# Performance work log

Hardware: AMD Instinct MI355X
Metric: run time of the kernel (lower is better)

## Reference

```python
import jax, jax.numpy as jnp
import numpy as np


def setup_inputs() -> dict:
    key = jax.random.key(0)
    k1, k2, k3 = jax.random.split(key, 3)
    N, C_in, H, W = 32, 16, 256, 256
    C_out, K = 64, 3
    x = jax.random.normal(k1, (N, C_in, H, W), dtype=jnp.float32)
    # match nn.Conv2d default init scale roughly (values irrelevant for correctness harness)
    fan_in = C_in * K * K
    bound = 1.0 / np.sqrt(fan_in)
    conv_weight = jax.random.normal(k2, (C_out, C_in, K, K), dtype=jnp.float32) * bound
    conv_bias = jax.random.normal(k3, (C_out,), dtype=jnp.float32) * bound
    return {"x": x, "conv_weight": conv_weight, "conv_bias": conv_bias}


def reference(x, conv_weight, conv_bias):
    # Conv2d: stride=1, padding=0 (VALID), dilation=1, groups=1
    y = jax.lax.conv_general_dilated(
        x, conv_weight,
        window_strides=(1, 1), padding='VALID',
        dimension_numbers=('NCHW', 'OIHW', 'NCHW'),
    ) + conv_bias[None, :, None, None]          # (N, C_out, OH, OW)
    y = jnp.min(y, axis=1, keepdims=True)       # min over output channels -> (N, 1, OH, OW)
    return jnp.tanh(jnp.tanh(y))                # double tanh
```

## Files before the change

kernel.cpp:

```cpp
#include <hip/hip_runtime.h>
#include <hip/hip_bf16.h>

typedef __attribute__((ext_vector_type(8)))  short short8;
typedef __attribute__((ext_vector_type(4)))  float f32x4;
typedef __attribute__((ext_vector_type(16))) float f32x16;

#define CIN   16
#define COUT  64
#define HH    256
#define WW    256
#define OHH   254
#define OWW   254

#define HSTR   (36 * 8)
#define HALF   (34 * HSTR + 8)

__device__ __forceinline__ ushort f2bf(float f) {
    unsigned u = __builtin_bit_cast(unsigned, f);
    unsigned r = (u + 0x7fffu + ((u >> 16) & 1u)) >> 16;
    return (ushort)r;
}

__device__ __forceinline__ float dtanh2(float x) {
    const float K = 2.8853900817779268f;
    float xc = fminf(fmaxf(x, -9.0f), 9.0f);
    float e1 = __builtin_amdgcn_exp2f(K * xc);
    float t1 = 1.0f - 2.0f * __builtin_amdgcn_rcpf(e1 + 1.0f);
    float e2 = __builtin_amdgcn_exp2f(K * t1);
    return 1.0f - 2.0f * __builtin_amdgcn_rcpf(e2 + 1.0f);
}

__global__ void prep_weights(const float* __restrict__ wsrc, ushort* __restrict__ wfrag) {
    int idx = blockIdx.x * 256 + threadIdx.x;
    if (idx >= 9216) return;
    int r    = idx & 7;
    int lane = (idx >> 3) & 63;
    int j    = (idx >> 9) & 1;
    int tap  = idx >> 10;
    int ci   = 8 * (lane >> 5) + r;
    int co   = j * 32 + (lane & 31);
    int kh   = tap / 3, kw = tap - 3 * kh;
    wfrag[idx] = f2bf(wsrc[(co * CIN + ci) * 9 + kh * 3 + kw]);
}

__global__ __launch_bounds__(256, 3) void conv_min_tanh(
        const float* __restrict__ x, const ushort* __restrict__ wfrag,
        const float* __restrict__ bias, float* __restrict__ out) {
    __shared__ ushort lds[2 * HALF];

    const int tid = threadIdx.x;
    const int n   = blockIdx.z;
    const int oh0 = blockIdx.y * 32;
    const int ow0 = blockIdx.x * 32;
    const int HW  = HH * WW;

    const float* xb = x + (size_t)n * CIN * HW;
    auto stage_pos = [&](int pos) {
        int hp  = pos / 36;
        int r2  = pos - hp * 36;
        int ciq = r2 / 9;
        int w4  = r2 - ciq * 9;
        int hg  = min(oh0 + hp, HH - 1);
        int wg  = min(ow0 + 4 * w4, WW - 4);
        const float* src = xb + (size_t)(ciq * 4) * HW + hg * WW + wg;
        f32x4 v0 = *reinterpret_cast<const f32x4*>(src);
        f32x4 v1 = *reinterpret_cast<const f32x4*>(src + HW);
        f32x4 v2 = *reinterpret_cast<const f32x4*>(src + 2 * HW);
        f32x4 v3 = *reinterpret_cast<const f32x4*>(src + 3 * HW);
        ushort* dst = &lds[(ciq >> 1) * HALF + (hp * 36 + 4 * w4) * 8 + (ciq & 1) * 4];
#pragma unroll
        for (int e = 0; e < 4; ++e) {
            unsigned lo, hi;
            asm("v_cvt_pk_bf16_f32 %0, %1, %2" : "=v"(lo) : "v"(v0[e]), "v"(v1[e]));
            asm("v_cvt_pk_bf16_f32 %0, %1, %2" : "=v"(hi) : "v"(v2[e]), "v"(v3[e]));
            uint2 pk; pk.x = lo; pk.y = hi;
            *reinterpret_cast<uint2*>(dst + e * 8) = pk;
        }
    };
#pragma unroll
    for (int it = 0; it < 4; ++it) stage_pos(tid + it * 256);
    if (tid < 1224 - 1024) stage_pos(tid + 1024);

    const int lane  = tid & 63;
    const int wid   = tid >> 6;
    const int px    = lane & 31;
    const int khalf = lane >> 5;

    short8 wf[9][2];
#pragma unroll
    for (int tap = 0; tap < 9; ++tap) {
        wf[tap][0] = *reinterpret_cast<const short8*>(wfrag + ((tap * 2 + 0) * 64 + lane) * 8);
        wf[tap][1] = *reinterpret_cast<const short8*>(wfrag + ((tap * 2 + 1) * 64 + lane) * 8);
    }
    f32x16 bi0, bi1;
#pragma unroll
    for (int q = 0; q < 4; ++q) {
        f32x4 b0 = *reinterpret_cast<const f32x4*>(bias +  0 + 4 * khalf + 8 * q);
        f32x4 b1 = *reinterpret_cast<const f32x4*>(bias + 32 + 4 * khalf + 8 * q);
#pragma unroll
        for (int s = 0; s < 4; ++s) { bi0[q * 4 + s] = b0[s]; bi1[q * 4 + s] = b1[s]; }
    }

    const ushort* bp[9];
#pragma unroll
    for (int tap = 0; tap < 9; ++tap) {
        int kh = tap / 3, kw = tap - 3 * kh;
        bp[tap] = &lds[khalf * HALF + (wid * 8 + kh) * HSTR + (px + kw) * 8];
    }

    __syncthreads();

#pragma unroll
    for (int i = 0; i < 8; ++i) {
        f32x16 a0 = bi0, a1 = bi1;
#pragma unroll
        for (int tap = 0; tap < 9; ++tap) {
            short8 b = *reinterpret_cast<const short8*>(bp[tap] + i * HSTR);
            a0 = __builtin_amdgcn_mfma_f32_32x32x16_bf16(wf[tap][0], b, a0, 0, 0, 0);
            a1 = __builtin_amdgcn_mfma_f32_32x32x16_bf16(wf[tap][1], b, a1, 0, 0, 0);
        }
        float v = fminf(a0[0], a1[0]);
#pragma unroll
        for (int r = 1; r < 16; ++r) v = fminf(v, fminf(a0[r], a1[r]));
        v = fminf(v, __shfl_xor(v, 32, 64));
        const float y  = dtanh2(v);
        const int   oh = oh0 + wid * 8 + i;
        const int   ow = ow0 + px;
        if (lane < 32 && oh < OHH && ow < OWW)
            out[((size_t)n * OHH + oh) * OWW + ow] = y;
    }
}

extern "C" void kernel_launch(void* const* d_in, const int* in_sizes, int n_in,
                              void* d_out, int out_size, void* d_ws, size_t ws_size,
                              hipStream_t stream) {
    const float* x = (const float*)d_in[0];
    const float* w = (const float*)d_in[1];
    const float* b = (const float*)d_in[2];
    float* out     = (float*)d_out;
    ushort* wfrag  = (ushort*)d_ws;

    prep_weights<<<36, 256, 0, stream>>>(w, wfrag);
    dim3 grid(8, 8, 32);
    conv_min_tanh<<<grid, dim3(256, 1, 1), 0, stream>>>(x, wfrag, b, out);
}
```

Before: 63.30 us.

## Process four images per block with double-buffered LDS prefetch of next tile

Each block now handles four batch images instead of one. While MFMA compute runs on the current image, the next image's input tile is loaded through inline-asm global loads into registers, then converted to bf16 into a second LDS buffer. The aim is to hide global load latency behind compute and to amortise the weight and bias fragment loads across images. In exchange, LDS use doubles, occupancy drops to 2 blocks per CU, register pressure rises from holding 80 floats of prefetch, and the grid shrinks to 512 blocks.

```diff
diff --git a/kernel.cpp b/kernel.cpp
--- a/kernel.cpp
+++ b/kernel.cpp
@@ -14,6 +14,7 @@
 
 #define HSTR   (36 * 8)
 #define HALF   (34 * HSTR + 8)
+#define BUFU   (2 * HALF)
 
 __device__ __forceinline__ ushort f2bf(float f) {
     unsigned u = __builtin_bit_cast(unsigned, f);
@@ -43,43 +44,61 @@
     wfrag[idx] = f2bf(wsrc[(co * CIN + ci) * 9 + kh * 3 + kw]);
 }
 
-__global__ __launch_bounds__(256, 3) void conv_min_tanh(
+__global__ __launch_bounds__(256, 2) void conv_min_tanh(
         const float* __restrict__ x, const ushort* __restrict__ wfrag,
         const float* __restrict__ bias, float* __restrict__ out) {
-    __shared__ ushort lds[2 * HALF];
+    __shared__ ushort lds[2 * BUFU];
 
     const int tid = threadIdx.x;
-    const int n   = blockIdx.z;
     const int oh0 = blockIdx.y * 32;
     const int ow0 = blockIdx.x * 32;
+    const int n0  = blockIdx.z * 4;
     const int HW  = HH * WW;
 
-    const float* xb = x + (size_t)n * CIN * HW;
-    auto stage_pos = [&](int pos) {
+    int goff[5], loff[5];
+#pragma unroll
+    for (int s = 0; s < 5; ++s) {
+        int pos = tid + s * 256;
+        if (pos > 1223) pos = 1223;
         int hp  = pos / 36;
         int r2  = pos - hp * 36;
         int ciq = r2 / 9;
         int w4  = r2 - ciq * 9;
         int hg  = min(oh0 + hp, HH - 1);
         int wg  = min(ow0 + 4 * w4, WW - 4);
-        const float* src = xb + (size_t)(ciq * 4) * HW + hg * WW + wg;
-        f32x4 v0 = *reinterpret_cast<const f32x4*>(src);
-        f32x4 v1 = *reinterpret_cast<const f32x4*>(src + HW);
-        f32x4 v2 = *reinterpret_cast<const f32x4*>(src + 2 * HW);
-        f32x4 v3 = *reinterpret_cast<const f32x4*>(src + 3 * HW);
-        ushort* dst = &lds[(ciq >> 1) * HALF + (hp * 36 + 4 * w4) * 8 + (ciq & 1) * 4];
+        goff[s] = (ciq * 4) * HW + hg * WW + wg;
+        loff[s] = (ciq >> 1) * HALF + (hp * 36 + 4 * w4) * 8 + (ciq & 1) * 4;
+    }
+
+    f32x4 r[5][4];
+    auto issue_loads = [&](const float* xb) {
 #pragma unroll
-        for (int e = 0; e < 4; ++e) {
-            unsigned lo, hi;
-            asm("v_cvt_pk_bf16_f32 %0, %1, %2" : "=v"(lo) : "v"(v0[e]), "v"(v1[e]));
-            asm("v_cvt_pk_bf16_f32 %0, %1, %2" : "=v"(hi) : "v"(v2[e]), "v"(v3[e]));
-            uint2 pk; pk.x = lo; pk.y = hi;
-            *reinterpret_cast<uint2*>(dst + e * 8) = pk;
+        for (int s = 0; s < 5; ++s) {
+            const float* p = xb + goff[s];
+            asm volatile("global_load_dwordx4 %0, %1, off"
+                         : "=v"(r[s][0]) : "v"(p) : "memory");
+            asm volatile("global_load_dwordx4 %0, %1, off"
+                         : "=v"(r[s][1]) : "v"(p + HW) : "memory");
+            asm volatile("global_load_dwordx4 %0, %1, off"
+                         : "=v"(r[s][2]) : "v"(p + 2 * HW) : "memory");
+            asm volatile("global_load_dwordx4 %0, %1, off"
+                         : "=v"(r[s][3]) : "v"(p + 3 * HW) : "memory");
         }
     };
+    auto write_all = [&](int base) {
 #pragma unroll
-    for (int it = 0; it < 4; ++it) stage_pos(tid + it * 256);
-    if (tid < 1224 - 1024) stage_pos(tid + 1024);
+        for (int s = 0; s < 5; ++s) {
+            ushort* dst = &lds[base + loff[s]];
+#pragma unroll
+            for (int e = 0; e < 4; ++e) {
+                unsigned lo, hi;
+                asm("v_cvt_pk_bf16_f32 %0, %1, %2" : "=v"(lo) : "v"(r[s][0][e]), "v"(r[s][1][e]));
+                asm("v_cvt_pk_bf16_f32 %0, %1, %2" : "=v"(hi) : "v"(r[s][2][e]), "v"(r[s][3][e]));
+                uint2 pk; pk.x = lo; pk.y = hi;
+                *reinterpret_cast<uint2*>(dst + e * 8) = pk;
+            }
+        }
+    };
 
     const int lane  = tid & 63;
     const int wid   = tid >> 6;
@@ -101,33 +120,51 @@
         for (int s = 0; s < 4; ++s) { bi0[q * 4 + s] = b0[s]; bi1[q * 4 + s] = b1[s]; }
     }
 
-    const ushort* bp[9];
+    int boff[9];
 #pragma unroll
     for (int tap = 0; tap < 9; ++tap) {
         int kh = tap / 3, kw = tap - 3 * kh;
-        bp[tap] = &lds[khalf * HALF + (wid * 8 + kh) * HSTR + (px + kw) * 8];
+        boff[tap] = khalf * HALF + (wid * 8 + kh) * HSTR + (px + kw) * 8;
     }
 
+    auto compute = [&](int base, int n) {
+#pragma unroll
+        for (int i = 0; i < 8; ++i) {
+            f32x16 a0 = bi0, a1 = bi1;
+#pragma unroll
+            for (int tap = 0; tap < 9; ++tap) {
+                short8 b = *reinterpret_cast<const short8*>(&lds[base + boff[tap] + i * HSTR]);
+                a0 = __builtin_amdgcn_mfma_f32_32x32x16_bf16(wf[tap][0], b, a0, 0, 0, 0);
+                a1 = __builtin_amdgcn_mfma_f32_32x32x16_bf16(wf[tap][1], b, a1, 0, 0, 0);
+            }
+            float v = fminf(a0[0], a1[0]);
+#pragma unroll
+            for (int q = 1; q < 16; ++q) v = fminf(v, fminf(a0[q], a1[q]));
+            v = fminf(v, __shfl_xor(v, 32, 64));
+            const float y  = dtanh2(v);
+            const int   oh = oh0 + wid * 8 + i;
+            const int   ow = ow0 + px;
+            if (lane < 32 && oh < OHH && ow < OWW)
+                out[((size_t)n * OHH + oh) * OWW + ow] = y;
+        }
+    };
+
+    issue_loads(x + (size_t)n0 * CIN * HW);
+    asm volatile("s_waitcnt vmcnt(0)" ::: "memory");
+    write_all(0);
     __syncthreads();
-
+    int cur = 0;
 #pragma unroll
-    for (int i = 0; i < 8; ++i) {
-        f32x16 a0 = bi0, a1 = bi1;
-#pragma unroll
-        for (int tap = 0; tap < 9; ++tap) {
-            short8 b = *reinterpret_cast<const short8*>(bp[tap] + i * HSTR);
-            a0 = __builtin_amdgcn_mfma_f32_32x32x16_bf16(wf[tap][0], b, a0, 0, 0, 0);
-            a1 = __builtin_amdgcn_mfma_f32_32x32x16_bf16(wf[tap][1], b, a1, 0, 0, 0);
+    for (int t = 0; t < 4; ++t) {
+        if (t < 3)
+            issue_loads(x + (size_t)(n0 + t + 1) * CIN * HW);
+        compute(cur * BUFU, n0 + t);
+        if (t < 3) {
+            asm volatile("s_waitcnt vmcnt(0)" ::: "memory");
+            write_all((cur ^ 1) * BUFU);
         }
-        float v = fminf(a0[0], a1[0]);
-#pragma unroll
-        for (int r = 1; r < 16; ++r) v = fminf(v, fminf(a0[r], a1[r]));
-        v = fminf(v, __shfl_xor(v, 32, 64));
-        const float y  = dtanh2(v);
-        const int   oh = oh0 + wid * 8 + i;
-        const int   ow = ow0 + px;
-        if (lane < 32 && oh < OHH && ow < OWW)
-            out[((size_t)n * OHH + oh) * OWW + ow] = y;
+        __syncthreads();
+        cur ^= 1;
     }
 }
 
@@ -141,6 +178,6 @@
     ushort* wfrag  = (ushort*)d_ws;
 
     prep_weights<<<36, 256, 0, stream>>>(w, wfrag);
-    dim3 grid(8, 8, 32);
+    dim3 grid(8, 8, 8);
     conv_min_tanh<<<grid, dim3(256, 1, 1), 0, stream>>>(x, wfrag, b, out);
 }
```

Result: slower. 70.22 us (+10.9%).

## Stream fp32 input rows into LDS via async global_load_lds triple buffering

Applied to the files above, without the earlier changes.

Input staging switches from register loads with bf16 conversion before the LDS write to direct global-to-LDS async loads of fp32 data in 8-row chunks. The chunks go into a three-buffer ring with an XOR swizzle, and each chunk is refilled while the previous one is computed. Conversion to bf16 now happens after the LDS read, right before each MFMA. The aim is to overlap global loads with MFMA work and remove the register round-trip in staging. The cost is double the LDS footprint (fp32), more conversion instructions in the inner loop, and a lower occupancy target (2 blocks per CU instead of 3).

```diff
diff --git a/kernel.cpp b/kernel.cpp
--- a/kernel.cpp
+++ b/kernel.cpp
@@ -6,20 +6,18 @@
 typedef __attribute__((ext_vector_type(16))) float f32x16;
 
 #define CIN   16
-#define COUT  64
 #define HH    256
 #define WW    256
 #define OHH   254
 #define OWW   254
+#define HW    (HH * WW)
 
-#define HSTR   (36 * 8)
-#define HALF   (34 * HSTR + 8)
+#define ROWB   2304
+#define CHUNKB 18432
 
-__device__ __forceinline__ ushort f2bf(float f) {
-    unsigned u = __builtin_bit_cast(unsigned, f);
-    unsigned r = (u + 0x7fffu + ((u >> 16) & 1u)) >> 16;
-    return (ushort)r;
-}
+#define GLOAD4(gp, lp) __builtin_amdgcn_global_load_lds( \
+    (const __attribute__((address_space(1))) void*)(gp), \
+    (__attribute__((address_space(3))) void*)(lp), 4, 0, 0)
 
 __device__ __forceinline__ float dtanh2(float x) {
     const float K = 2.8853900817779268f;
@@ -28,6 +26,12 @@
     float t1 = 1.0f - 2.0f * __builtin_amdgcn_rcpf(e1 + 1.0f);
     float e2 = __builtin_amdgcn_exp2f(K * t1);
     return 1.0f - 2.0f * __builtin_amdgcn_rcpf(e2 + 1.0f);
+}
+
+__device__ __forceinline__ ushort f2bf(float f) {
+    unsigned u = __builtin_bit_cast(unsigned, f);
+    unsigned r = (u + 0x7fffu + ((u >> 16) & 1u)) >> 16;
+    return (ushort)r;
 }
 
 __global__ void prep_weights(const float* __restrict__ wsrc, ushort* __restrict__ wfrag) {
@@ -43,49 +47,68 @@
     wfrag[idx] = f2bf(wsrc[(co * CIN + ci) * 9 + kh * 3 + kw]);
 }
 
-__global__ __launch_bounds__(256, 3) void conv_min_tanh(
+__global__ __launch_bounds__(256, 2) void conv_min_tanh(
         const float* __restrict__ x, const ushort* __restrict__ wfrag,
         const float* __restrict__ bias, float* __restrict__ out) {
-    __shared__ ushort lds[2 * HALF];
+    __shared__ __attribute__((aligned(64))) char lds[3 * CHUNKB];
 
-    const int tid = threadIdx.x;
-    const int n   = blockIdx.z;
-    const int oh0 = blockIdx.y * 32;
-    const int ow0 = blockIdx.x * 32;
-    const int HW  = HH * WW;
+    const int tid  = threadIdx.x;
+    const int lane = tid & 63;
+    const int wid  = tid >> 6;
+    const int n    = blockIdx.z;
+    const int oh0  = blockIdx.y * 32;
+    const int ow0  = blockIdx.x * 32;
+    const float* xb = x + ((size_t)n << 20);
 
-    const float* xb = x + (size_t)n * CIN * HW;
-    auto stage_pos = [&](int pos) {
-        int hp  = pos / 36;
-        int r2  = pos - hp * 36;
-        int ciq = r2 / 9;
-        int w4  = r2 - ciq * 9;
-        int hg  = min(oh0 + hp, HH - 1);
-        int wg  = min(ow0 + 4 * w4, WW - 4);
-        const float* src = xb + (size_t)(ciq * 4) * HW + hg * WW + wg;
-        f32x4 v0 = *reinterpret_cast<const f32x4*>(src);
-        f32x4 v1 = *reinterpret_cast<const f32x4*>(src + HW);
-        f32x4 v2 = *reinterpret_cast<const f32x4*>(src + 2 * HW);
-        f32x4 v3 = *reinterpret_cast<const f32x4*>(src + 3 * HW);
-        ushort* dst = &lds[(ciq >> 1) * HALF + (hp * 36 + 4 * w4) * 8 + (ciq & 1) * 4];
+    auto decode = [&](int o) -> unsigned {
+        int b  = o * 4;
+        int L  = b ^ (((b >> 6) & 3) << 4);
+        int rs = L / ROWB;
+        int rem = L - rs * ROWB;
+        int w  = rem >> 6;
+        int ci = (rem & 63) >> 2;
+        int wg = min(ow0 + w, WW - 1);
+        return ((unsigned)rs << 24) | ((unsigned)ci << 16) | (unsigned)wg;
+    };
+    unsigned pkk[18];
 #pragma unroll
-        for (int e = 0; e < 4; ++e) {
-            unsigned lo, hi;
-            asm("v_cvt_pk_bf16_f32 %0, %1, %2" : "=v"(lo) : "v"(v0[e]), "v"(v1[e]));
-            asm("v_cvt_pk_bf16_f32 %0, %1, %2" : "=v"(hi) : "v"(v2[e]), "v"(v3[e]));
-            uint2 pk; pk.x = lo; pk.y = hi;
-            *reinterpret_cast<uint2*>(dst + e * 8) = pk;
+    for (int k = 0; k < 18; ++k)
+        pkk[k] = decode((wid * 18 + k) * 64 + lane);
+    const int mstart = wid * 5 - (wid > 2 ? 1 : 0) - (wid > 3 ? 1 : 0);
+    const int mcnt   = (wid < 2) ? 5 : 4;
+    unsigned pmini[5];
+#pragma unroll
+    for (int k = 0; k < 5; ++k)
+        pmini[k] = decode((mstart + min(k, mcnt - 1)) * 64 + lane);
+
+    auto refill = [&](int c) {
+        const int rowbase = oh0 + 8 * c + 2;
+        char* lbase = lds + (c % 3) * CHUNKB + wid * 4608;
+#pragma unroll
+        for (int k = 0; k < 18; ++k) {
+            unsigned pk = pkk[k];
+            int hg = min(rowbase + (int)(pk >> 24), HH - 1);
+            const float* g = xb + ((pk & 0xFFFFFFu) + (hg << 8));
+            GLOAD4(g, lbase + k * 256);
         }
     };
+
+    refill(0);
+    {
+        char* lbase = lds + 2 * CHUNKB + mstart * 256;
 #pragma unroll
-    for (int it = 0; it < 4; ++it) stage_pos(tid + it * 256);
-    if (tid < 1224 - 1024) stage_pos(tid + 1024);
+        for (int k = 0; k < 5; ++k) {
+            if (k < mcnt) {
+                unsigned pk = pmini[k];
+                int hg = oh0 + (int)(pk >> 24);
+                const float* g = xb + ((pk & 0xFFFFFFu) + (hg << 8));
+                GLOAD4(g, lbase + k * 256);
+            }
+        }
+    }
 
-    const int lane  = tid & 63;
-    const int wid   = tid >> 6;
     const int px    = lane & 31;
     const int khalf = lane >> 5;
-
     short8 wf[9][2];
 #pragma unroll
     for (int tap = 0; tap < 9; ++tap) {
@@ -94,40 +117,70 @@
     }
     f32x16 bi0, bi1;
 #pragma unroll
-    for (int q = 0; q < 4; ++q) {
-        f32x4 b0 = *reinterpret_cast<const f32x4*>(bias +  0 + 4 * khalf + 8 * q);
-        f32x4 b1 = *reinterpret_cast<const f32x4*>(bias + 32 + 4 * khalf + 8 * q);
+    for (int q4 = 0; q4 < 4; ++q4) {
+        f32x4 b0 = *reinterpret_cast<const f32x4*>(bias +  0 + 4 * khalf + 8 * q4);
+        f32x4 b1 = *reinterpret_cast<const f32x4*>(bias + 32 + 4 * khalf + 8 * q4);
 #pragma unroll
-        for (int s = 0; s < 4; ++s) { bi0[q * 4 + s] = b0[s]; bi1[q * 4 + s] = b1[s]; }
+        for (int s = 0; s < 4; ++s) { bi0[q4 * 4 + s] = b0[s]; bi1[q4 * 4 + s] = b1[s]; }
+    }
+    int colv[3], colh[3];
+#pragma unroll
+    for (int kw = 0; kw < 3; ++kw) {
+        int c = (px + kw) * 64 + khalf * 32;
+        int X = ((px + kw) & 3) << 4;
+        colv[kw] = c ^ X;
+        colh[kw] = (c + 16) ^ X;
     }
 
-    const ushort* bp[9];
-#pragma unroll
-    for (int tap = 0; tap < 9; ++tap) {
-        int kh = tap / 3, kw = tap - 3 * kh;
-        bp[tap] = &lds[khalf * HALF + (wid * 8 + kh) * HSTR + (px + kw) * 8];
-    }
-
+    asm volatile("s_waitcnt vmcnt(0)" ::: "memory");
     __syncthreads();
 
 #pragma unroll
-    for (int i = 0; i < 8; ++i) {
-        f32x16 a0 = bi0, a1 = bi1;
+    for (int q = 0; q < 4; ++q) {
+        if (q < 3) refill(q + 1);
+
+        const char* curb  = lds + (q % 3) * CHUNKB;
+        const char* prevb = lds + ((q + 2) % 3) * CHUNKB;
 #pragma unroll
-        for (int tap = 0; tap < 9; ++tap) {
-            short8 b = *reinterpret_cast<const short8*>(bp[tap] + i * HSTR);
-            a0 = __builtin_amdgcn_mfma_f32_32x32x16_bf16(wf[tap][0], b, a0, 0, 0, 0);
-            a1 = __builtin_amdgcn_mfma_f32_32x32x16_bf16(wf[tap][1], b, a1, 0, 0, 0);
+        for (int jj = 0; jj < 2; ++jj) {
+            f32x16 a0 = bi0, a1 = bi1;
+#pragma unroll
+            for (int kh = 0; kh < 3; ++kh) {
+                const int t = jj + kh;
+                const int p_rel = 2 * wid + t;
+                const char* rb;
+                if (p_rel < 2) {
+                    rb = (q == 0) ? prevb + p_rel * ROWB
+                                  : prevb + (6 + p_rel) * ROWB;
+                } else {
+                    rb = curb + (p_rel - 2) * ROWB;
+                }
+#pragma unroll
+                for (int kw = 0; kw < 3; ++kw) {
+                    f32x4 lo = *reinterpret_cast<const f32x4*>(rb + colv[kw]);
+                    f32x4 hi = *reinterpret_cast<const f32x4*>(rb + colh[kw]);
+                    unsigned d0, d1, d2, d3;
+                    asm("v_cvt_pk_bf16_f32 %0, %1, %2" : "=v"(d0) : "v"(lo[0]), "v"(lo[1]));
+                    asm("v_cvt_pk_bf16_f32 %0, %1, %2" : "=v"(d1) : "v"(lo[2]), "v"(lo[3]));
+                    asm("v_cvt_pk_bf16_f32 %0, %1, %2" : "=v"(d2) : "v"(hi[0]), "v"(hi[1]));
+                    asm("v_cvt_pk_bf16_f32 %0, %1, %2" : "=v"(d3) : "v"(hi[2]), "v"(hi[3]));
+                    union { unsigned u[4]; short8 s; } fb = {{d0, d1, d2, d3}};
+                    a0 = __builtin_amdgcn_mfma_f32_32x32x16_bf16(wf[kh * 3 + kw][0], fb.s, a0, 0, 0, 0);
+                    a1 = __builtin_amdgcn_mfma_f32_32x32x16_bf16(wf[kh * 3 + kw][1], fb.s, a1, 0, 0, 0);
+                }
+            }
+            float v = fminf(a0[0], a1[0]);
+#pragma unroll
+            for (int r = 1; r < 16; ++r) v = fminf(v, fminf(a0[r], a1[r]));
+            v = fminf(v, __shfl_xor(v, 32, 64));
+            const float y  = dtanh2(v);
+            const int   oh = oh0 + 8 * q + 2 * wid + jj;
+            const int   ow = ow0 + px;
+            if (lane < 32 && oh < OHH && ow < OWW)
+                out[((size_t)n * OHH + oh) * OWW + ow] = y;
         }
-        float v = fminf(a0[0], a1[0]);
-#pragma unroll
-        for (int r = 1; r < 16; ++r) v = fminf(v, fminf(a0[r], a1[r]));
-        v = fminf(v, __shfl_xor(v, 32, 64));
-        const float y  = dtanh2(v);
-        const int   oh = oh0 + wid * 8 + i;
-        const int   ow = ow0 + px;
-        if (lane < 32 && oh < OHH && ow < OWW)
-            out[((size_t)n * OHH + oh) * OWW + ow] = y;
+        asm volatile("s_waitcnt vmcnt(0)" ::: "memory");
+        __syncthreads();
     }
 }
 
```

New measurement: 100.2 us. 1.58x slower.

## Split output channels across waves and reduce min through LDS

Applied to the files above, without the earlier changes.

Each wave now computes one 32-channel half for 16 output rows instead of both halves for 8 rows. This halves the per-wave weight fragments and accumulators, so occupancy can rise to 4 blocks per CU. Partial minima are exchanged through LDS as bf16, combined, passed through the double tanh, and written with vectorized float4 stores. The extra barriers add cost, and storing the pre-activation minima in bf16 adds rounding error.

```diff
diff --git a/kernel.cpp b/kernel.cpp
--- a/kernel.cpp
+++ b/kernel.cpp
@@ -6,7 +6,6 @@
 typedef __attribute__((ext_vector_type(16))) float f32x16;
 
 #define CIN   16
-#define COUT  64
 #define HH    256
 #define WW    256
 #define OHH   254
@@ -43,7 +42,7 @@
     wfrag[idx] = f2bf(wsrc[(co * CIN + ci) * 9 + kh * 3 + kw]);
 }
 
-__global__ __launch_bounds__(256, 3) void conv_min_tanh(
+__global__ __launch_bounds__(256, 4) void conv_min_tanh(
         const float* __restrict__ x, const ushort* __restrict__ wfrag,
         const float* __restrict__ bias, float* __restrict__ out) {
     __shared__ ushort lds[2 * HALF];
@@ -83,51 +82,78 @@
 
     const int lane  = tid & 63;
     const int wid   = tid >> 6;
+    const int jw    = wid & 1;
+    const int rh    = wid >> 1;
     const int px    = lane & 31;
     const int khalf = lane >> 5;
 
-    short8 wf[9][2];
+    short8 wf[9];
 #pragma unroll
-    for (int tap = 0; tap < 9; ++tap) {
-        wf[tap][0] = *reinterpret_cast<const short8*>(wfrag + ((tap * 2 + 0) * 64 + lane) * 8);
-        wf[tap][1] = *reinterpret_cast<const short8*>(wfrag + ((tap * 2 + 1) * 64 + lane) * 8);
+    for (int tap = 0; tap < 9; ++tap)
+        wf[tap] = *reinterpret_cast<const short8*>(wfrag + ((tap * 2 + jw) * 64 + lane) * 8);
+    f32x16 bi;
+#pragma unroll
+    for (int q4 = 0; q4 < 4; ++q4) {
+        f32x4 b = *reinterpret_cast<const f32x4*>(bias + jw * 32 + 4 * khalf + 8 * q4);
+#pragma unroll
+        for (int s = 0; s < 4; ++s) bi[q4 * 4 + s] = b[s];
     }
-    f32x16 bi0, bi1;
-#pragma unroll
-    for (int q = 0; q < 4; ++q) {
-        f32x4 b0 = *reinterpret_cast<const f32x4*>(bias +  0 + 4 * khalf + 8 * q);
-        f32x4 b1 = *reinterpret_cast<const f32x4*>(bias + 32 + 4 * khalf + 8 * q);
-#pragma unroll
-        for (int s = 0; s < 4; ++s) { bi0[q * 4 + s] = b0[s]; bi1[q * 4 + s] = b1[s]; }
-    }
-
     const ushort* bp[9];
 #pragma unroll
     for (int tap = 0; tap < 9; ++tap) {
         int kh = tap / 3, kw = tap - 3 * kh;
-        bp[tap] = &lds[khalf * HALF + (wid * 8 + kh) * HSTR + (px + kw) * 8];
+        bp[tap] = &lds[khalf * HALF + (rh * 16 + kh) * HSTR + (px + kw) * 8];
     }
 
     __syncthreads();
 
+    float mv[16];
 #pragma unroll
-    for (int i = 0; i < 8; ++i) {
-        f32x16 a0 = bi0, a1 = bi1;
+    for (int i = 0; i < 16; ++i) {
+        f32x16 a = bi;
 #pragma unroll
         for (int tap = 0; tap < 9; ++tap) {
             short8 b = *reinterpret_cast<const short8*>(bp[tap] + i * HSTR);
-            a0 = __builtin_amdgcn_mfma_f32_32x32x16_bf16(wf[tap][0], b, a0, 0, 0, 0);
-            a1 = __builtin_amdgcn_mfma_f32_32x32x16_bf16(wf[tap][1], b, a1, 0, 0, 0);
+            a = __builtin_amdgcn_mfma_f32_32x32x16_bf16(wf[tap], b, a, 0, 0, 0);
         }
-        float v = fminf(a0[0], a1[0]);
+        float v = a[0];
 #pragma unroll
-        for (int r = 1; r < 16; ++r) v = fminf(v, fminf(a0[r], a1[r]));
+        for (int r = 1; r < 16; ++r) v = fminf(v, a[r]);
         v = fminf(v, __shfl_xor(v, 32, 64));
-        const float y  = dtanh2(v);
-        const int   oh = oh0 + wid * 8 + i;
-        const int   ow = ow0 + px;
-        if (lane < 32 && oh < OHH && ow < OWW)
-            out[((size_t)n * OHH + oh) * OWW + ow] = y;
+        mv[i] = v;
+    }
+
+    __syncthreads();
+
+    if (lane < 32) {
+#pragma unroll
+        for (int i = 0; i < 16; ++i)
+            lds[(jw * 32 + rh * 16 + i) * 32 + px] = f2bf(mv[i]);
+    }
+    __syncthreads();
+
+    const int row = tid >> 3, px4 = (tid & 7) * 4;
+    uint2 p0 = *reinterpret_cast<const uint2*>(&lds[(     row) * 32 + px4]);
+    uint2 p1 = *reinterpret_cast<const uint2*>(&lds[(32 + row) * 32 + px4]);
+    f32x4 y;
+#pragma unroll
+    for (int e = 0; e < 4; ++e) {
+        unsigned w0 = (e < 2) ? p0.x : p0.y;
+        unsigned w1 = (e < 2) ? p1.x : p1.y;
+        float f0 = __builtin_bit_cast(float, (e & 1) ? (w0 & 0xffff0000u) : (w0 << 16));
+        float f1 = __builtin_bit_cast(float, (e & 1) ? (w1 & 0xffff0000u) : (w1 << 16));
+        y[e] = dtanh2(fminf(f0, f1));
+    }
+    const int oh = oh0 + row, ow = ow0 + px4;
+    if (oh < OHH) {
+        float* op = &out[((size_t)n * OHH + oh) * OWW + ow];
+        if (ow + 3 < OWW) {
+            *reinterpret_cast<f32x4*>(op) = y;
+        } else {
+#pragma unroll
+            for (int e = 0; e < 4; ++e)
+                if (ow + e < OWW) op[e] = y[e];
+        }
     }
 }
 
```

Measured after the change: 57.66 us. 1.1x faster.
